# Kernel optimization log

Hardware: AMD Instinct MI355X
Metric: run time of the kernel (lower is better)

The kernel has to match this reference:

```python
import jax, jax.numpy as jnp
import numpy as np

IH, IW = 256, 704
FH, FW = 32, 88
D_MIN, D_MAX, D_RES = 1.0, 60.0, 0.5
D = int(np.ceil((D_MAX - D_MIN) / D_RES))  # 118 depth bins
C_IN, HID, C_OUT = 256, 64, 80
N_R, N_THETA = 128, 256
BN_EPS = 1e-5


def _edges():
    # non-uniform polar grid: angular bins uniform, radial bins grow with r
    ang = np.linspace(-np.pi / 2, np.pi / 2, N_THETA + 1).astype(np.float32)
    t = np.linspace(0.0, 1.0, N_R + 1)
    rad = (D_MIN + (t ** 1.5) * (D_MAX - D_MIN)).astype(np.float32)
    return jnp.asarray(ang), jnp.asarray(rad)


def _frustum():
    # [D, fH, fW, 3] of (u, v, depth) samples in image space
    ds = np.arange(D_MIN, D_MAX, D_RES, dtype=np.float32)
    xs = np.linspace(0, IW - 1, FW, dtype=np.float32)
    ys = np.linspace(0, IH - 1, FH, dtype=np.float32)
    d = np.broadcast_to(ds[:, None, None], (D, FH, FW))
    x = np.broadcast_to(xs[None, None, :], (D, FH, FW))
    y = np.broadcast_to(ys[None, :, None], (D, FH, FW))
    return jnp.asarray(np.stack([x, y, d], axis=-1))


def _bn(x, g, b, m, v):
    # inference-mode BatchNorm2d over channel axis 1; x: [BN, C, H, W]
    inv = g / jnp.sqrt(v + BN_EPS)
    return x * inv[None, :, None, None] + (b - m * inv)[None, :, None, None]


def setup_inputs() -> dict:
    key = jax.random.key(0)
    ks = jax.random.split(key, 8)
    B, N = 2, 1
    x = jax.random.normal(ks[0], (B, N, C_IN, FH, FW), dtype=jnp.float32)
    # camera->lidar axis permutation: x_l = z_c, y_l = -x_c, z_l = -y_c
    R = jnp.asarray([[0.0, 0.0, 1.0], [-1.0, 0.0, 0.0], [0.0, -1.0, 0.0]], dtype=jnp.float32)
    camera2lidar_rots = jnp.broadcast_to(R, (B, N, 3, 3))
    camera2lidar_trans = jnp.zeros((B, N, 3), dtype=jnp.float32)
    K = jnp.asarray([[380.0, 0.0, IW / 2.0], [0.0, 380.0, IH / 2.0], [0.0, 0.0, 1.0]], dtype=jnp.float32)
    intrins = jnp.broadcast_to(K, (B, N, 3, 3))
    s = 0.02
    params = dict(
        w1=jax.random.normal(ks[1], (HID, C_IN), dtype=jnp.float32) * s,
        b1=jnp.zeros((HID,), dtype=jnp.float32),
        g1=jnp.ones((HID,), dtype=jnp.float32),
        be1=jnp.zeros((HID,), dtype=jnp.float32),
        m1=jax.random.normal(ks[2], (HID,), dtype=jnp.float32) * s,
        v1=jnp.abs(jax.random.normal(ks[3], (HID,), dtype=jnp.float32)) + 0.5,
        w2=jax.random.normal(ks[4], (D + C_OUT, HID), dtype=jnp.float32) * s,
        b2=jnp.zeros((D + C_OUT,), dtype=jnp.float32),
        g2=jnp.ones((D + C_OUT,), dtype=jnp.float32),
        be2=jnp.zeros((D + C_OUT,), dtype=jnp.float32),
        m2=jax.random.normal(ks[5], (D + C_OUT,), dtype=jnp.float32) * s,
        v2=jnp.abs(jax.random.normal(ks[6], (D + C_OUT,), dtype=jnp.float32)) + 0.5,
    )
    return dict(x=x, camera2lidar_rots=camera2lidar_rots,
                camera2lidar_trans=camera2lidar_trans, intrins=intrins, **params)


def reference(x, camera2lidar_rots, camera2lidar_trans, intrins,
              w1, b1, g1, be1, m1, v1, w2, b2, g2, be2, m2, v2):
    B, N = x.shape[0], x.shape[1]
    # --- LIFT: DepthNet (two 1x1 convs + BN) -> depth dist x features outer product ---
    xf = x.reshape(B * N, C_IN, FH, FW)
    h = jnp.einsum('bchw,oc->bohw', xf, w1) + b1[None, :, None, None]
    h = jax.nn.relu(_bn(h, g1, be1, m1, v1))
    h = jnp.einsum('bchw,oc->bohw', h, w2) + b2[None, :, None, None]
    h = _bn(h, g2, be2, m2, v2)
    depth = jax.nn.softmax(h[:, :D], axis=1)            # [BN, D, fH, fW]
    feat = h[:, D:D + C_OUT]                            # [BN, C, fH, fW]
    lifted = depth[:, None, :, :, :] * feat[:, :, None, :, :]   # [BN, C, D, fH, fW]
    lifted = lifted.reshape(B, N, C_OUT, D, FH, FW).transpose(0, 1, 3, 4, 5, 2)  # [B,N,D,fH,fW,C]

    # --- geometry: unproject frustum to lidar frame ---
    fr = _frustum()                                      # [D, fH, fW, 3]
    u, v_, d = fr[..., 0], fr[..., 1], fr[..., 2]
    fx = intrins[..., 0, 0][:, :, None, None, None]
    fy = intrins[..., 1, 1][:, :, None, None, None]
    cx = intrins[..., 0, 2][:, :, None, None, None]
    cy = intrins[..., 1, 2][:, :, None, None, None]
    pc = jnp.stack([(u - cx) * d / fx, (v_ - cy) * d / fy,
                    jnp.broadcast_to(d, (B, N, D, FH, FW))], axis=-1)  # [B,N,D,fH,fW,3]
    pts = jnp.einsum('bnij,bndhwj->bndhwi', camera2lidar_rots, pc)
    pts = pts + camera2lidar_trans[:, :, None, None, None, :]

    # --- SPLAT: scatter-sum into non-uniform polar BEV grid ---
    ang_e, rad_e = _edges()
    xl, yl = pts[..., 0], pts[..., 1]
    r = jnp.sqrt(xl * xl + yl * yl)
    th = jnp.arctan2(yl, xl)
    r_idx = jnp.searchsorted(rad_e, r, side='right') - 1   # non-uniform bins -> bucketize
    t_idx = jnp.searchsorted(ang_e, th, side='right') - 1
    valid = (r_idx >= 0) & (r_idx < N_R) & (t_idx >= 0) & (t_idx < N_THETA)
    b_idx = jnp.arange(B)[:, None, None, None, None]
    trash = B * N_R * N_THETA  # dummy segment for out-of-grid points
    seg = jnp.where(valid, (b_idx * N_R + r_idx) * N_THETA + t_idx, trash).reshape(-1)
    bev = jax.ops.segment_sum(lifted.reshape(-1, C_OUT), seg, num_segments=trash + 1)[:-1]
    bev = bev.reshape(B, N_R, N_THETA, C_OUT).transpose(0, 3, 1, 2)  # [B, C, n_r, n_theta]
    return bev
```

## Files before the change

### kernel.cpp

```cpp
#include <hip/hip_runtime.h>
#include <hip/hip_bf16.h>
#include <math.h>

#define FH 32
#define FW 88
#define DD 118
#define C_IN 256
#define HID 64
#define C_OUT 80
#define NPIX 5632
#define PIX_PER_B 2816
#define N_R 128
#define N_THETA 256
#define NCOL 176
#define NBIN 32768
#define ECAP 12
#define PSTRIDE 9440

typedef __attribute__((ext_vector_type(8))) short short8;
typedef __attribute__((ext_vector_type(4))) float f32x4;

__device__ inline float bf2f(unsigned short h) {
  return __uint_as_float((unsigned)h << 16);
}
__device__ inline unsigned short f2bf(float f) {
  unsigned u = __float_as_uint(f);
  unsigned r = (u + 0x7fffu + ((u >> 16) & 1u)) >> 16;
  return (unsigned short)r;
}
__device__ inline bool detect_bf16(const void* intr) {
  float f = __uint_as_float(*(const unsigned*)intr);
  return !(f > 300.0f && f < 500.0f);
}
__device__ inline float ldf(const void* p, int i, bool isb) {
  return isb ? bf2f(((const unsigned short*)p)[i]) : ((const float*)p)[i];
}

__device__ inline void load_geom(int tid, float* radEL, float* angEL, float* camsL,
                                 const void* rots, const void* trans, const void* intr,
                                 bool isb) {
  if (tid < 129) {
    double t = (double)tid * (1.0 / 128.0);
    radEL[tid] = (float)(1.0 + pow(t, 1.5) * 59.0);
  }
  for (int i = tid; i < 257; i += 256) {
    double step = M_PI / 256.0;
    double vv = (i == 256) ? (M_PI / 2.0) : ((double)i * step + (-M_PI / 2.0));
    angEL[i] = (float)vv;
  }
  if (tid < 18) camsL[tid] = ldf(rots, tid, isb);
  if (tid < 6)  camsL[20 + tid] = ldf(trans, tid, isb);
  if (tid >= 6 && tid < 24) camsL[28 + (tid - 6)] = ldf(intr, tid - 6, isb);
}

__device__ inline int computeBin(int w, int h, int d,
                                 const float* camsF, int b,
                                 const float* radE, const float* angE) {
  float fx = camsF[28 + b * 9 + 0], cx = camsF[28 + b * 9 + 2];
  float fy = camsF[28 + b * 9 + 4], cy = camsF[28 + b * 9 + 5];
  float R00 = camsF[b * 9 + 0], R01 = camsF[b * 9 + 1], R02 = camsF[b * 9 + 2];
  float R10 = camsF[b * 9 + 3], R11 = camsF[b * 9 + 4], R12 = camsF[b * 9 + 5];
  float Tx = camsF[20 + b * 3 + 0], Ty = camsF[20 + b * 3 + 1];
  float u  = (w == FW - 1) ? 703.0f : (float)((double)w * (703.0 / 87.0));
  float vv = (h == FH - 1) ? 255.0f : (float)((double)h * (255.0 / 31.0));
  float dd = 1.0f + 0.5f * (float)d;
  float px = __fdiv_rn(__fmul_rn(__fsub_rn(u, cx), dd), fx);
  float py = __fdiv_rn(__fmul_rn(__fsub_rn(vv, cy), dd), fy);
  float xl = __fadd_rn(__fadd_rn(__fadd_rn(__fmul_rn(R00, px), __fmul_rn(R01, py)),
                                 __fmul_rn(R02, dd)), Tx);
  float yl = __fadd_rn(__fadd_rn(__fadd_rn(__fmul_rn(R10, px), __fmul_rn(R11, py)),
                                 __fmul_rn(R12, dd)), Ty);
  float r = __fsqrt_rn(__fadd_rn(__fmul_rn(xl, xl), __fmul_rn(yl, yl)));
  float th = (float)atan2((double)yl, (double)xl);
  int lo = 0, hi = 129;
  while (lo < hi) { int mid = (lo + hi) >> 1; if (radE[mid] <= r) lo = mid + 1; else hi = mid; }
  int ri = lo - 1;
  lo = 0; hi = 257;
  while (lo < hi) { int mid = (lo + hi) >> 1; if (angE[mid] <= th) lo = mid + 1; else hi = mid; }
  int ti = lo - 1;
  bool valid = (ri >= 0) && (ri < N_R) && (ti >= 0) && (ti < N_THETA);
  return valid ? (ri * N_THETA + ti) : -1;
}


__device__ __forceinline__ void dev_mlp(
    int pix0, int tid, float* shbuf, float* h1L,
    float* inv1L, float* b1fL, float* inv2L, float* b2fL,
    const void* __restrict__ xraw,
    const void* __restrict__ w1r, const void* __restrict__ b1r,
    const void* __restrict__ g1r, const void* __restrict__ be1r,
    const void* __restrict__ m1r, const void* __restrict__ v1r,
    const void* __restrict__ w2r, const void* __restrict__ b2r,
    const void* __restrict__ g2r, const void* __restrict__ be2r,
    const void* __restrict__ m2r, const void* __restrict__ v2r,
    float* __restrict__ depthW, float* __restrict__ featW, bool isb) {
  unsigned short* xsU = (unsigned short*)shbuf;
  float* h2s = shbuf;
  float* smaxL = shbuf + 3200;
  float* ssumL = shbuf + 3456;
  if (tid < 64) {
    float iv = ldf(g1r, tid, isb) / sqrtf(ldf(v1r, tid, isb) + 1e-5f);
    inv1L[tid] = iv;
    b1fL[tid] = ldf(b1r, tid, isb) * iv + (ldf(be1r, tid, isb) - ldf(m1r, tid, isb) * iv);
  }
  if (tid < 198) {
    float iv = ldf(g2r, tid, isb) / sqrtf(ldf(v2r, tid, isb) + 1e-5f);
    inv2L[tid] = iv;
    b2fL[tid] = ldf(b2r, tid, isb) * iv + (ldf(be2r, tid, isb) - ldf(m2r, tid, isb) * iv);
  }
  int b = pix0 / PIX_PER_B;
  int ploc0 = pix0 - b * PIX_PER_B;
  size_t xbase = (size_t)b * C_IN * PIX_PER_B + ploc0;
  const unsigned short* xh = (const unsigned short*)xraw;
  const float* xf = (const float*)xraw;
  {
    int p = tid & 15, crow = tid >> 4;
    for (int it = 0; it < 16; it++) {
      int c = it * 16 + crow;
      size_t gi = xbase + (size_t)c * PIX_PER_B + p;
      xsU[p * 264 + c] = isb ? xh[gi] : f2bf(xf[gi]);
    }
  }
  int lane = tid & 63, wv = tid >> 6;
  int nloc = lane & 15, quad = lane >> 4;
  int orow = wv * 16 + nloc;
  short8 afr[8];
  const unsigned short* w1h = (const unsigned short*)w1r;
  const float* w1f32 = (const float*)w1r;
  if (isb) {
#pragma unroll
    for (int s = 0; s < 8; s++)
      afr[s] = *(const short8*)(w1h + orow * 256 + s * 32 + quad * 8);
  } else {
#pragma unroll
    for (int s = 0; s < 8; s++) {
      short8 a;
#pragma unroll
      for (int j = 0; j < 8; j++)
        a[j] = (short)f2bf(w1f32[orow * 256 + s * 32 + quad * 8 + j]);
      afr[s] = a;
    }
  }
  __syncthreads();
  f32x4 acc = {0.f, 0.f, 0.f, 0.f};
#pragma unroll
  for (int s = 0; s < 8; s++) {
    short8 bfr = *(const short8*)(xsU + nloc * 264 + s * 32 + quad * 8);
    acc = __builtin_amdgcn_mfma_f32_16x16x32_bf16(afr[s], bfr, acc, 0, 0, 0);
  }
#pragma unroll
  for (int r = 0; r < 4; r++) {
    int mm = wv * 16 + quad * 4 + r;
    float hv = fmaxf(fmaf(acc[r], inv1L[mm], b1fL[mm]), 0.f);
    h1L[nloc * 68 + mm] = hv;
  }
  __syncthreads();
  int p = tid & 15, g = tid >> 4;
  float h1v[64];
  const float4* hp = (const float4*)(h1L + p * 68);
#pragma unroll
  for (int k4 = 0; k4 < 16; k4++) {
    float4 hv = hp[k4];
    h1v[4 * k4 + 0] = hv.x; h1v[4 * k4 + 1] = hv.y;
    h1v[4 * k4 + 2] = hv.z; h1v[4 * k4 + 3] = hv.w;
  }
  for (int j = 0; j < 13; j++) {
    int o = g * 13 + j;
    if (o < 198) {
      float iv = inv2L[o];
      float q0 = 0.f, q1 = 0.f, q2 = 0.f, q3 = 0.f;
      if (isb) {
        const ushort4* wr = (const ushort4*)w2r;
#pragma unroll
        for (int k4 = 0; k4 < 16; k4 += 4) {
          ushort4 u0 = wr[o * 16 + k4 + 0];
          ushort4 u1 = wr[o * 16 + k4 + 1];
          ushort4 u2 = wr[o * 16 + k4 + 2];
          ushort4 u3 = wr[o * 16 + k4 + 3];
          q0 = fmaf(bf2f(u0.x) * iv, h1v[4 * k4 + 0], q0);
          q0 = fmaf(bf2f(u0.y) * iv, h1v[4 * k4 + 1], q0);
          q0 = fmaf(bf2f(u0.z) * iv, h1v[4 * k4 + 2], q0);
          q0 = fmaf(bf2f(u0.w) * iv, h1v[4 * k4 + 3], q0);
          q1 = fmaf(bf2f(u1.x) * iv, h1v[4 * k4 + 4], q1);
          q1 = fmaf(bf2f(u1.y) * iv, h1v[4 * k4 + 5], q1);
          q1 = fmaf(bf2f(u1.z) * iv, h1v[4 * k4 + 6], q1);
          q1 = fmaf(bf2f(u1.w) * iv, h1v[4 * k4 + 7], q1);
          q2 = fmaf(bf2f(u2.x) * iv, h1v[4 * k4 + 8], q2);
          q2 = fmaf(bf2f(u2.y) * iv, h1v[4 * k4 + 9], q2);
          q2 = fmaf(bf2f(u2.z) * iv, h1v[4 * k4 + 10], q2);
          q2 = fmaf(bf2f(u2.w) * iv, h1v[4 * k4 + 11], q2);
          q3 = fmaf(bf2f(u3.x) * iv, h1v[4 * k4 + 12], q3);
          q3 = fmaf(bf2f(u3.y) * iv, h1v[4 * k4 + 13], q3);
          q3 = fmaf(bf2f(u3.z) * iv, h1v[4 * k4 + 14], q3);
          q3 = fmaf(bf2f(u3.w) * iv, h1v[4 * k4 + 15], q3);
        }
      } else {
        const float4* wr = (const float4*)w2r;
#pragma unroll
        for (int k4 = 0; k4 < 16; k4 += 4) {
          float4 w0 = wr[o * 16 + k4 + 0];
          float4 w1v = wr[o * 16 + k4 + 1];
          float4 w2v = wr[o * 16 + k4 + 2];
          float4 w3v = wr[o * 16 + k4 + 3];
          q0 = fmaf(w0.x * iv, h1v[4 * k4 + 0], q0);
          q0 = fmaf(w0.y * iv, h1v[4 * k4 + 1], q0);
          q0 = fmaf(w0.z * iv, h1v[4 * k4 + 2], q0);
          q0 = fmaf(w0.w * iv, h1v[4 * k4 + 3], q0);
          q1 = fmaf(w1v.x * iv, h1v[4 * k4 + 4], q1);
          q1 = fmaf(w1v.y * iv, h1v[4 * k4 + 5], q1);
          q1 = fmaf(w1v.z * iv, h1v[4 * k4 + 6], q1);
          q1 = fmaf(w1v.w * iv, h1v[4 * k4 + 7], q1);
          q2 = fmaf(w2v.x * iv, h1v[4 * k4 + 8], q2);
          q2 = fmaf(w2v.y * iv, h1v[4 * k4 + 9], q2);
          q2 = fmaf(w2v.z * iv, h1v[4 * k4 + 10], q2);
          q2 = fmaf(w2v.w * iv, h1v[4 * k4 + 11], q2);
          q3 = fmaf(w3v.x * iv, h1v[4 * k4 + 12], q3);
          q3 = fmaf(w3v.y * iv, h1v[4 * k4 + 13], q3);
          q3 = fmaf(w3v.z * iv, h1v[4 * k4 + 14], q3);
          q3 = fmaf(w3v.w * iv, h1v[4 * k4 + 15], q3);
        }
      }
      h2s[o * 16 + p] = b2fL[o] + ((q0 + q1) + (q2 + q3));
    }
  }
  __syncthreads();
  int r0 = g * 8, r1 = min(118, r0 + 8);
  float lm = -INFINITY;
  for (int o = r0; o < r1; o++) lm = fmaxf(lm, h2s[o * 16 + p]);
  smaxL[g * 16 + p] = lm;
  __syncthreads();
  float m = smaxL[p];
#pragma unroll
  for (int gg = 1; gg < 16; gg++) m = fmaxf(m, smaxL[gg * 16 + p]);
  float ls = 0.f;
  for (int o = r0; o < r1; o++) ls += expf(h2s[o * 16 + p] - m);
  ssumL[g * 16 + p] = ls;
  __syncthreads();
  float tot = 0.f;
#pragma unroll
  for (int gg = 0; gg < 16; gg++) tot += ssumL[gg * 16 + p];
  int pix = pix0 + p;
  for (int o = r0; o < r1; o++)
    depthW[(size_t)pix * DD + o] = expf(h2s[o * 16 + p] - m) / tot;
  int f0 = g * 5;
  for (int f = f0; f < f0 + 5; f++)
    featW[(size_t)pix * C_OUT + f] = h2s[(118 + f) * 16 + p];
}

__device__ __forceinline__ void dev_bins(
    int blk_rel, int tid, float* radEL, float* angEL, float* camsL,
    const void* rots, const void* trans, const void* intr, bool isb,
    int* __restrict__ cnt, unsigned* __restrict__ ent, int* __restrict__ flag) {
  int t = blk_rel * 256 + tid;
  load_geom(tid, radEL, angEL, camsL, rots, trans, intr, isb);
  __syncthreads();
  if (t < NCOL * DD) {
    int col = t / DD, d = t - col * DD;
    int b = col / FW, w = col - b * FW;
    float R01 = camsL[b * 9 + 1], R11 = camsL[b * 9 + 4];
    if (!(R01 == 0.0f && R11 == 0.0f)) atomicOr(flag, 1);
    int bin = computeBin(w, 0, d, camsL, b, radEL, angEL);
    if (bin >= 0) {
      int slot = atomicAdd(&cnt[b * NBIN + bin], 1);
      if (slot < ECAP) ent[(size_t)(b * NBIN + bin) * ECAP + slot] = ((unsigned)col << 8) | (unsigned)d;
      else atomicOr(flag, 1);
    }
  }
}

__device__ __forceinline__ void dev_pcol(
    int col, int tid, float* depthL, float* featL,
    const float* __restrict__ depthW, const float* __restrict__ featW,
    float* __restrict__ P) {
  int b = col / FW, w = col - b * FW;
  size_t colPix = (size_t)b * PIX_PER_B + w;
  for (int i = tid; i < FH * DD; i += 256) {
    int h = i / DD, d = i - h * DD;
    depthL[h * 120 + d] = depthW[(colPix + (size_t)h * FW) * DD + d];
  }
  for (int i = tid; i < FH * C_OUT; i += 256) {
    int h = i / C_OUT, c = i - h * C_OUT;
    featL[i] = featW[(colPix + (size_t)h * FW) * C_OUT + c];
  }
  __syncthreads();
  const float4* featL4 = (const float4*)featL;
  const float4* depthL4 = (const float4*)depthL;
  float4* P4 = (float4*)(P + (size_t)col * PSTRIDE);
  for (int t = tid; t < 30 * 20; t += 256) {
    int dq = t / 20, c4 = t - dq * 20;
    float4 a0 = make_float4(0.f, 0.f, 0.f, 0.f);
    float4 a1 = make_float4(0.f, 0.f, 0.f, 0.f);
    float4 a2 = make_float4(0.f, 0.f, 0.f, 0.f);
    float4 a3 = make_float4(0.f, 0.f, 0.f, 0.f);
#pragma unroll
    for (int h = 0; h < FH; h++) {
      float4 wd = depthL4[h * 30 + dq];
      float4 f = featL4[h * 20 + c4];
      a0.x = fmaf(wd.x, f.x, a0.x); a0.y = fmaf(wd.x, f.y, a0.y);
      a0.z = fmaf(wd.x, f.z, a0.z); a0.w = fmaf(wd.x, f.w, a0.w);
      a1.x = fmaf(wd.y, f.x, a1.x); a1.y = fmaf(wd.y, f.y, a1.y);
      a1.z = fmaf(wd.y, f.z, a1.z); a1.w = fmaf(wd.y, f.w, a1.w);
      a2.x = fmaf(wd.z, f.x, a2.x); a2.y = fmaf(wd.z, f.y, a2.y);
      a2.z = fmaf(wd.z, f.z, a2.z); a2.w = fmaf(wd.z, f.w, a2.w);
      a3.x = fmaf(wd.w, f.x, a3.x); a3.y = fmaf(wd.w, f.y, a3.y);
      a3.z = fmaf(wd.w, f.z, a3.z); a3.w = fmaf(wd.w, f.w, a3.w);
    }
    int d0 = dq * 4;
    P4[(d0 + 0) * 20 + c4] = a0;
    P4[(d0 + 1) * 20 + c4] = a1;
    if (d0 + 2 < DD) {
      P4[(d0 + 2) * 20 + c4] = a2;
      P4[(d0 + 3) * 20 + c4] = a3;
    }
  }
}

__device__ __forceinline__ void dev_scatter(
    int idx2, int tid, float* depthL, float* featL,
    float* radEL, float* angEL, float* camsL,
    const void* rots, const void* trans, const void* intr, bool isb,
    const float* __restrict__ depthW, const float* __restrict__ featW,
    float* __restrict__ bevAcc) {
  int col = idx2 >> 1, chalf = idx2 & 1;
  int b = col / FW, w = col - b * FW;
  load_geom(tid, radEL, angEL, camsL, rots, trans, intr, isb);
  size_t colPix = (size_t)b * PIX_PER_B + w;
  for (int i = tid; i < FH * DD; i += 256) {
    int h = i / DD, d = i - h * DD;
    depthL[d * 33 + h] = depthW[(colPix + (size_t)h * FW) * DD + d];
  }
  for (int i = tid; i < FH * C_OUT; i += 256) {
    int h = i / C_OUT, c = i - h * C_OUT;
    featL[i] = featW[(colPix + (size_t)h * FW) * C_OUT + c];
  }
  __syncthreads();
  const float4* featL4 = (const float4*)featL;
  for (int t = tid; t < DD * FH * 10; t += 256) {
    int d = t / 320, rem = t - d * 320;
    int h = rem / 10, c4 = chalf * 10 + (rem - (rem / 10) * 10);
    int bin = computeBin(w, h, d, camsL, b, radEL, angEL);
    if (bin < 0) continue;
    float wd = depthL[d * 33 + h];
    float4 f = featL4[h * 20 + c4];
    float* outb = bevAcc + (((size_t)(b * C_OUT + c4 * 4)) << 15) + bin;
    unsafeAtomicAdd(outb, wd * f.x);
    unsafeAtomicAdd(outb + (1u << 15), wd * f.y);
    unsafeAtomicAdd(outb + (2u << 15), wd * f.z);
    unsafeAtomicAdd(outb + (3u << 15), wd * f.w);
  }
}

__device__ __forceinline__ void dev_out_main(
    int vt, int tid, const float* __restrict__ P,
    const int* __restrict__ cnt, const unsigned* __restrict__ ent,
    void* __restrict__ out, bool isb) {
  int b = vt >> 7;
  int ri = vt & 127;
  int bin = ri * N_THETA + tid;
  int n = cnt[b * NBIN + bin];
  if (n > ECAP) n = ECAP;
  unsigned ee[ECAP];
  const unsigned* eb = ent + (size_t)(b * NBIN + bin) * ECAP;
  for (int i = 0; i < n; i++) ee[i] = eb[i];
  for (int i = 1; i < n; i++) {
    unsigned key = ee[i]; int j = i - 1;
    while (j >= 0 && ee[j] > key) { ee[j + 1] = ee[j]; j--; }
    ee[j + 1] = key;
  }
  int base[ECAP];
  for (int i = 0; i < n; i++)
    base[i] = (int)(((ee[i] >> 8) * PSTRIDE + (ee[i] & 255u) * C_OUT) >> 2);
  const float4* P4 = (const float4*)P;
  unsigned short* oh = (unsigned short*)out;
  float* of = (float*)out;
  size_t obase = (((size_t)(b * C_OUT)) << 15) + bin;
  for (int c4 = 0; c4 < 20; c4++) {
    float4 s = make_float4(0.f, 0.f, 0.f, 0.f);
    for (int i = 0; i < n; i++) {
      float4 v = P4[base[i] + c4];
      s.x += v.x; s.y += v.y; s.z += v.z; s.w += v.w;
    }
    size_t o0 = obase + ((size_t)(c4 * 4) << 15);
    if (isb) {
      oh[o0]              = f2bf(s.x);
      oh[o0 + (1u << 15)] = f2bf(s.y);
      oh[o0 + (2u << 15)] = f2bf(s.z);
      oh[o0 + (3u << 15)] = f2bf(s.w);
    } else {
      of[o0]              = s.x;
      of[o0 + (1u << 15)] = s.y;
      of[o0 + (2u << 15)] = s.z;
      of[o0 + (3u << 15)] = s.w;
    }
  }
}

__device__ __forceinline__ void dev_out_copy(
    int gtid, int gstride, const float* __restrict__ bevAcc,
    void* __restrict__ out, bool isb) {
  const float4* a4 = (const float4*)bevAcc;
  int n4 = (NBIN * 2 * C_OUT) / 4;
  if (isb) {
    ushort4* o4 = (ushort4*)out;
    for (int i = gtid; i < n4; i += gstride) {
      float4 v = a4[i];
      ushort4 o; o.x = f2bf(v.x); o.y = f2bf(v.y); o.z = f2bf(v.z); o.w = f2bf(v.w);
      o4[i] = o;
    }
  } else {
    float4* o4 = (float4*)out;
    for (int i = gtid; i < n4; i += gstride) o4[i] = a4[i];
  }
}


__global__ __launch_bounds__(256) void k_mlp(
    const void* __restrict__ xraw,
    const void* __restrict__ w1r, const void* __restrict__ b1r,
    const void* __restrict__ g1r, const void* __restrict__ be1r,
    const void* __restrict__ m1r, const void* __restrict__ v1r,
    const void* __restrict__ w2r, const void* __restrict__ b2r,
    const void* __restrict__ g2r, const void* __restrict__ be2r,
    const void* __restrict__ m2r, const void* __restrict__ v2r,
    const void* __restrict__ intr,
    float* __restrict__ depthW, float* __restrict__ featW) {
  __shared__ __align__(16) float shbuf[3712];
  __shared__ __align__(16) float h1L[16 * 68];
  __shared__ float inv1L[64], b1fL[64], inv2L[198], b2fL[198];
  bool isb = detect_bf16(intr);
  dev_mlp(blockIdx.x * 16, threadIdx.x, shbuf, h1L, inv1L, b1fL, inv2L, b2fL,
          xraw, w1r, b1r, g1r, be1r, m1r, v1r,
          w2r, b2r, g2r, be2r, m2r, v2r, depthW, featW, isb);
}

__global__ __launch_bounds__(256) void k_bins(
    const void* __restrict__ rots, const void* __restrict__ trans,
    const void* __restrict__ intr,
    int* __restrict__ cnt, unsigned* __restrict__ ent, int* __restrict__ flag) {
  __shared__ float radEL[129], angEL[257], camsL[46];
  bool isb = detect_bf16(intr);
  dev_bins(blockIdx.x, threadIdx.x, radEL, angEL, camsL,
           rots, trans, intr, isb, cnt, ent, flag);
}

__global__ __launch_bounds__(256) void k_pcol(
    const float* __restrict__ depthW, const float* __restrict__ featW,
    const int* __restrict__ flag, float* __restrict__ P) {
  __shared__ __align__(16) float depthL[32 * 120];
  __shared__ __align__(16) float featL[FH * C_OUT];
  if (*flag != 0) return;
  dev_pcol(blockIdx.x, threadIdx.x, depthL, featL, depthW, featW, P);
}

__global__ __launch_bounds__(256) void k_zerofb(
    const int* __restrict__ flag, float* __restrict__ bevAcc) {
  if (*flag == 0) return;
  float4 z = make_float4(0.f, 0.f, 0.f, 0.f);
  float4* bz = (float4*)bevAcc;
  int n4 = (NBIN * 2 * C_OUT) / 4;
  for (int i = blockIdx.x * 256 + threadIdx.x; i < n4; i += 320 * 256) bz[i] = z;
}

__global__ __launch_bounds__(256) void k_scatter(
    const float* __restrict__ depthW, const float* __restrict__ featW,
    const int* __restrict__ flag,
    const void* __restrict__ rots, const void* __restrict__ trans,
    const void* __restrict__ intr, float* __restrict__ bevAcc) {
  __shared__ __align__(16) float depthL[DD * 33];
  __shared__ __align__(16) float featL[FH * C_OUT];
  __shared__ float radEL[129], angEL[257], camsL[46];
  if (*flag == 0) return;
  bool isb = detect_bf16(intr);
  dev_scatter(blockIdx.x, threadIdx.x, depthL, featL, radEL, angEL, camsL,
              rots, trans, intr, isb, depthW, featW, bevAcc);
}

__global__ __launch_bounds__(256) void k_outg(
    const float* __restrict__ P, const int* __restrict__ cnt,
    const unsigned* __restrict__ ent, const int* __restrict__ flag,
    void* __restrict__ out, const void* __restrict__ intrRaw) {
  if (*flag != 0) return;
  bool isb = detect_bf16(intrRaw);
  dev_out_main(blockIdx.x, threadIdx.x, P, cnt, ent, out, isb);
}

__global__ __launch_bounds__(256) void k_copy(
    const float* __restrict__ bevAcc, const int* __restrict__ flag,
    void* __restrict__ out, const void* __restrict__ intrRaw) {
  if (*flag == 0) return;
  bool isb = detect_bf16(intrRaw);
  dev_out_copy(blockIdx.x * 256 + threadIdx.x, 1024 * 256, bevAcc, out, isb);
}

extern "C" void kernel_launch(void* const* d_in, const int* in_sizes, int n_in,
                              void* d_out, int out_size, void* d_ws, size_t ws_size,
                              hipStream_t stream) {
  const void* x     = d_in[0];
  const void* rots  = d_in[1];
  const void* trans = d_in[2];
  const void* intr  = d_in[3];
  const void* w1  = d_in[4];
  const void* b1  = d_in[5];
  const void* g1  = d_in[6];
  const void* be1 = d_in[7];
  const void* m1  = d_in[8];
  const void* v1  = d_in[9];
  const void* w2  = d_in[10];
  const void* b2  = d_in[11];
  const void* g2  = d_in[12];
  const void* be2 = d_in[13];
  const void* m2  = d_in[14];
  const void* v2  = d_in[15];

  float* ws = (float*)d_ws;
  float*    P      = ws + 0;
  int*      cnt    = (int*)(ws + 1661440);
  int*      flag   = (int*)(ws + 1726976);
  unsigned* ent    = (unsigned*)(ws + 1727040);
  float*    depthW = ws + 2513472;
  float*    featW  = ws + 3178048;
  float*    bevAcc = ws + 3628608;

  (void)hipMemsetAsync(cnt, 0, (size_t)(65536 + 64) * sizeof(int), stream);

  k_mlp<<<352, 256, 0, stream>>>(x, w1, b1, g1, be1, m1, v1,
                                 w2, b2, g2, be2, m2, v2, intr, depthW, featW);
  k_bins<<<82, 256, 0, stream>>>(rots, trans, intr, cnt, ent, flag);
  k_pcol<<<NCOL, 256, 0, stream>>>(depthW, featW, flag, P);
  k_zerofb<<<320, 256, 0, stream>>>(flag, bevAcc);
  k_scatter<<<NCOL * 2, 256, 0, stream>>>(depthW, featW, flag, rots, trans, intr, bevAcc);
  k_outg<<<2 * N_R, 256, 0, stream>>>(P, cnt, ent, flag, d_out, intr);
  k_copy<<<1024, 256, 0, stream>>>(bevAcc, flag, d_out, intr);
}
```

Measured before the change: 154.1 us.

## Merge pipeline stages into four launches and split pcol/output work per block

Result: faster. 147.4 us (-4.3%).

```diff
diff --git a/kernel.cpp b/kernel.cpp
--- a/kernel.cpp
+++ b/kernel.cpp
@@ -268,15 +268,18 @@
   }
 }
 
-__device__ __forceinline__ void dev_pcol(
-    int col, int tid, float* depthL, float* featL,
+__device__ __forceinline__ void dev_pcol_half(
+    int col, int dhalf, int tid, float* depthL, float* featL,
     const float* __restrict__ depthW, const float* __restrict__ featW,
     float* __restrict__ P) {
   int b = col / FW, w = col - b * FW;
   size_t colPix = (size_t)b * PIX_PER_B + w;
-  for (int i = tid; i < FH * DD; i += 256) {
-    int h = i / DD, d = i - h * DD;
-    depthL[h * 120 + d] = depthW[(colPix + (size_t)h * FW) * DD + d];
+  int dbase = dhalf * 60;
+  for (int i = tid; i < FH * 60; i += 256) {
+    int h = i / 60, dloc = i - h * 60;
+    int d = dbase + dloc;
+    if (d < DD)
+      depthL[h * 60 + dloc] = depthW[(colPix + (size_t)h * FW) * DD + d];
   }
   for (int i = tid; i < FH * C_OUT; i += 256) {
     int h = i / C_OUT, c = i - h * C_OUT;
@@ -286,15 +289,16 @@
   const float4* featL4 = (const float4*)featL;
   const float4* depthL4 = (const float4*)depthL;
   float4* P4 = (float4*)(P + (size_t)col * PSTRIDE);
-  for (int t = tid; t < 30 * 20; t += 256) {
-    int dq = t / 20, c4 = t - dq * 20;
+  for (int t = tid; t < 15 * 20; t += 256) {
+    int lq = t / 20, c4 = t - lq * 20;
+    int dq = dhalf * 15 + lq;
     float4 a0 = make_float4(0.f, 0.f, 0.f, 0.f);
     float4 a1 = make_float4(0.f, 0.f, 0.f, 0.f);
     float4 a2 = make_float4(0.f, 0.f, 0.f, 0.f);
     float4 a3 = make_float4(0.f, 0.f, 0.f, 0.f);
 #pragma unroll
     for (int h = 0; h < FH; h++) {
-      float4 wd = depthL4[h * 30 + dq];
+      float4 wd = depthL4[h * 15 + lq];
       float4 f = featL4[h * 20 + c4];
       a0.x = fmaf(wd.x, f.x, a0.x); a0.y = fmaf(wd.x, f.y, a0.y);
       a0.z = fmaf(wd.x, f.z, a0.z); a0.w = fmaf(wd.x, f.w, a0.w);
@@ -350,8 +354,8 @@
   }
 }
 
-__device__ __forceinline__ void dev_out_main(
-    int vt, int tid, const float* __restrict__ P,
+__device__ __forceinline__ void dev_out_rng(
+    int vt, int tid, int c4lo, int c4hi, const float* __restrict__ P,
     const int* __restrict__ cnt, const unsigned* __restrict__ ent,
     void* __restrict__ out, bool isb) {
   int b = vt >> 7;
@@ -374,7 +378,7 @@
   unsigned short* oh = (unsigned short*)out;
   float* of = (float*)out;
   size_t obase = (((size_t)(b * C_OUT)) << 15) + bin;
-  for (int c4 = 0; c4 < 20; c4++) {
+  for (int c4 = c4lo; c4 < c4hi; c4++) {
     float4 s = make_float4(0.f, 0.f, 0.f, 0.f);
     for (int i = 0; i < n; i++) {
       float4 v = P4[base[i] + c4];
@@ -414,7 +418,7 @@
 }
 
 
-__global__ __launch_bounds__(256) void k_mlp(
+__global__ __launch_bounds__(256) void k_p1(
     const void* __restrict__ xraw,
     const void* __restrict__ w1r, const void* __restrict__ b1r,
     const void* __restrict__ g1r, const void* __restrict__ be1r,
@@ -423,68 +427,80 @@
     const void* __restrict__ g2r, const void* __restrict__ be2r,
     const void* __restrict__ m2r, const void* __restrict__ v2r,
     const void* __restrict__ intr,
-    float* __restrict__ depthW, float* __restrict__ featW) {
+    float* __restrict__ depthW, float* __restrict__ featW,
+    int* __restrict__ cnt, float* __restrict__ bevAcc) {
   __shared__ __align__(16) float shbuf[3712];
   __shared__ __align__(16) float h1L[16 * 68];
   __shared__ float inv1L[64], b1fL[64], inv2L[198], b2fL[198];
+  int tid = threadIdx.x;
+  if (blockIdx.x >= 352 + 16) {
+    int zb = blockIdx.x - (352 + 16);
+    float4 z = make_float4(0.f, 0.f, 0.f, 0.f);
+    float4* bz = (float4*)bevAcc;
+    int n4 = (NBIN * 2 * C_OUT) / 4;
+    for (int i = zb * 256 + tid; i < n4; i += 81 * 256) bz[i] = z;
+    return;
+  }
+  if (blockIdx.x >= 352) {
+    int zb = blockIdx.x - 352;
+    int4 z4 = make_int4(0, 0, 0, 0);
+    int4* c4p = (int4*)cnt;
+    for (int i = zb * 256 + tid; i < 16400; i += 16 * 256) c4p[i] = z4;
+    return;
+  }
   bool isb = detect_bf16(intr);
-  dev_mlp(blockIdx.x * 16, threadIdx.x, shbuf, h1L, inv1L, b1fL, inv2L, b2fL,
+  dev_mlp(blockIdx.x * 16, tid, shbuf, h1L, inv1L, b1fL, inv2L, b2fL,
           xraw, w1r, b1r, g1r, be1r, m1r, v1r,
           w2r, b2r, g2r, be2r, m2r, v2r, depthW, featW, isb);
 }
 
-__global__ __launch_bounds__(256) void k_bins(
+__global__ __launch_bounds__(256) void k_p2(
+    const float* __restrict__ depthW, const float* __restrict__ featW,
     const void* __restrict__ rots, const void* __restrict__ trans,
     const void* __restrict__ intr,
-    int* __restrict__ cnt, unsigned* __restrict__ ent, int* __restrict__ flag) {
+    int* __restrict__ cnt, unsigned* __restrict__ ent, int* __restrict__ flag,
+    float* __restrict__ P) {
+  __shared__ __align__(16) float depthL[32 * 60];
+  __shared__ __align__(16) float featL[FH * C_OUT];
   __shared__ float radEL[129], angEL[257], camsL[46];
+  int tid = threadIdx.x;
   bool isb = detect_bf16(intr);
-  dev_bins(blockIdx.x, threadIdx.x, radEL, angEL, camsL,
-           rots, trans, intr, isb, cnt, ent, flag);
-}
-
-__global__ __launch_bounds__(256) void k_pcol(
+  if (blockIdx.x >= 352) {
+    dev_bins(blockIdx.x - 352, tid, radEL, angEL, camsL,
+             rots, trans, intr, isb, cnt, ent, flag);
+    return;
+  }
+  if (*flag != 0) return;
+  dev_pcol_half(blockIdx.x >> 1, blockIdx.x & 1, tid, depthL, featL,
+                depthW, featW, P);
+}
+
+__global__ __launch_bounds__(256) void k_p3(
+    const float* __restrict__ P, const int* __restrict__ cnt,
+    const unsigned* __restrict__ ent, const int* __restrict__ flag,
     const float* __restrict__ depthW, const float* __restrict__ featW,
-    const int* __restrict__ flag, float* __restrict__ P) {
-  __shared__ __align__(16) float depthL[32 * 120];
-  __shared__ __align__(16) float featL[FH * C_OUT];
-  if (*flag != 0) return;
-  dev_pcol(blockIdx.x, threadIdx.x, depthL, featL, depthW, featW, P);
-}
-
-__global__ __launch_bounds__(256) void k_zerofb(
-    const int* __restrict__ flag, float* __restrict__ bevAcc) {
-  if (*flag == 0) return;
-  float4 z = make_float4(0.f, 0.f, 0.f, 0.f);
-  float4* bz = (float4*)bevAcc;
-  int n4 = (NBIN * 2 * C_OUT) / 4;
-  for (int i = blockIdx.x * 256 + threadIdx.x; i < n4; i += 320 * 256) bz[i] = z;
-}
-
-__global__ __launch_bounds__(256) void k_scatter(
-    const float* __restrict__ depthW, const float* __restrict__ featW,
-    const int* __restrict__ flag,
     const void* __restrict__ rots, const void* __restrict__ trans,
-    const void* __restrict__ intr, float* __restrict__ bevAcc) {
+    const void* __restrict__ intr,
+    float* __restrict__ bevAcc, void* __restrict__ out) {
   __shared__ __align__(16) float depthL[DD * 33];
   __shared__ __align__(16) float featL[FH * C_OUT];
   __shared__ float radEL[129], angEL[257], camsL[46];
-  if (*flag == 0) return;
+  int tid = threadIdx.x;
   bool isb = detect_bf16(intr);
-  dev_scatter(blockIdx.x, threadIdx.x, depthL, featL, radEL, angEL, camsL,
-              rots, trans, intr, isb, depthW, featW, bevAcc);
-}
-
-__global__ __launch_bounds__(256) void k_outg(
-    const float* __restrict__ P, const int* __restrict__ cnt,
-    const unsigned* __restrict__ ent, const int* __restrict__ flag,
-    void* __restrict__ out, const void* __restrict__ intrRaw) {
-  if (*flag != 0) return;
-  bool isb = detect_bf16(intrRaw);
-  dev_out_main(blockIdx.x, threadIdx.x, P, cnt, ent, out, isb);
-}
-
-__global__ __launch_bounds__(256) void k_copy(
+  int fl = *flag;
+  if (blockIdx.x >= 512) {
+    if (fl == 0) return;
+    dev_scatter(blockIdx.x - 512, tid, depthL, featL, radEL, angEL, camsL,
+                rots, trans, intr, isb, depthW, featW, bevAcc);
+    return;
+  }
+  if (fl != 0) return;
+  int half = blockIdx.x & 1;
+  dev_out_rng(blockIdx.x >> 1, tid, half * 10, half * 10 + 10,
+              P, cnt, ent, out, isb);
+}
+
+__global__ __launch_bounds__(256) void k_p4(
     const float* __restrict__ bevAcc, const int* __restrict__ flag,
     void* __restrict__ out, const void* __restrict__ intrRaw) {
   if (*flag == 0) return;
@@ -521,14 +537,12 @@
   float*    featW  = ws + 3178048;
   float*    bevAcc = ws + 3628608;
 
-  (void)hipMemsetAsync(cnt, 0, (size_t)(65536 + 64) * sizeof(int), stream);
-
-  k_mlp<<<352, 256, 0, stream>>>(x, w1, b1, g1, be1, m1, v1,
-                                 w2, b2, g2, be2, m2, v2, intr, depthW, featW);
-  k_bins<<<82, 256, 0, stream>>>(rots, trans, intr, cnt, ent, flag);
-  k_pcol<<<NCOL, 256, 0, stream>>>(depthW, featW, flag, P);
-  k_zerofb<<<320, 256, 0, stream>>>(flag, bevAcc);
-  k_scatter<<<NCOL * 2, 256, 0, stream>>>(depthW, featW, flag, rots, trans, intr, bevAcc);
-  k_outg<<<2 * N_R, 256, 0, stream>>>(P, cnt, ent, flag, d_out, intr);
-  k_copy<<<1024, 256, 0, stream>>>(bevAcc, flag, d_out, intr);
-}
+  k_p1<<<449, 256, 0, stream>>>(x, w1, b1, g1, be1, m1, v1,
+                                w2, b2, g2, be2, m2, v2, intr,
+                                depthW, featW, cnt, bevAcc);
+  k_p2<<<434, 256, 0, stream>>>(depthW, featW, rots, trans, intr,
+                                cnt, ent, flag, P);
+  k_p3<<<864, 256, 0, stream>>>(P, cnt, ent, flag, depthW, featW,
+                                rots, trans, intr, bevAcc, d_out);
+  k_p4<<<1024, 256, 0, stream>>>(bevAcc, flag, d_out, intr);
+}
```
